# Performance work log

Measured on AMD Instinct MI355X. Metric: run time of the kernel, lower is better.

Reference implementation:

```python
import jax, jax.numpy as jnp
import numpy as np

N_NODES = 100000
N_EDGES = 600000
H_FEATS = 128


def setup_inputs() -> dict:
    key = jax.random.key(0)
    k_h, k_src, k_dst, k_w1, k_w2 = jax.random.split(key, 5)
    h = jax.random.normal(k_h, (N_NODES, H_FEATS), dtype=jnp.float32)
    src = jax.random.randint(k_src, (N_EDGES,), 0, N_NODES, dtype=jnp.int64)
    dst = jax.random.randint(k_dst, (N_EDGES,), 0, N_NODES, dtype=jnp.int64)
    # torch.nn.Linear-style params: out = x @ W.T + b
    W1_w = jax.random.normal(k_w1, (H_FEATS, 2 * H_FEATS), dtype=jnp.float32) * (1.0 / np.sqrt(2 * H_FEATS))
    W1_b = jnp.zeros((H_FEATS,), dtype=jnp.float32)
    W2_w = jax.random.normal(k_w2, (1, H_FEATS), dtype=jnp.float32) * (1.0 / np.sqrt(H_FEATS))
    W2_b = jnp.zeros((1,), dtype=jnp.float32)
    return {"h": h, "src": src, "dst": dst, "W1_w": W1_w, "W1_b": W1_b, "W2_w": W2_w, "W2_b": W2_b}


def reference(h, src, dst, W1_w, W1_b, W2_w, W2_b):
    # Gather endpoint features per edge and concatenate: [E, 2*h_feats]
    edge_feat = jnp.concatenate([h[src], h[dst]], axis=-1)
    # 2-layer MLP per edge: Linear -> ReLU -> Linear, scalar score per edge
    hid = jax.nn.relu(edge_feat @ W1_w.T + W1_b)  # [E, h_feats]
    score = hid @ W2_w.T + W2_b                   # [E, 1]
    return score[:, 0]                            # [E]
```

## Files before the change

kernel.cpp:

```cpp
#include <hip/hip_runtime.h>
#include <hip/hip_bf16.h>
#include <stdint.h>

typedef short bf16x8 __attribute__((ext_vector_type(8)));
typedef float f32x4  __attribute__((ext_vector_type(4)));

__device__ __forceinline__ ushort f2b(float f) {
  __hip_bfloat16 t = __float2bfloat16(f);
  return *reinterpret_cast<ushort*>(&t);
}
__device__ __forceinline__ bf16x8 pack8(float4 a, float4 b) {
  bf16x8 r;
  r[0]=(short)f2b(a.x); r[1]=(short)f2b(a.y); r[2]=(short)f2b(a.z); r[3]=(short)f2b(a.w);
  r[4]=(short)f2b(b.x); r[5]=(short)f2b(b.y); r[6]=(short)f2b(b.z); r[7]=(short)f2b(b.w);
  return r;
}

__global__ void repack_W1(const float* __restrict__ W1, int4* __restrict__ blob) {
  const int tid = blockIdx.x * 256 + threadIdx.x;
  const int l15  = tid & 15;
  const int lg   = (tid >> 4) & 3;
  const int kk   = (tid >> 6) & 3;
  const int nt   = (tid >> 8) & 7;
  const int half = (tid >> 11) & 1;
  const float* wp = W1 + (size_t)(nt * 16 + l15) * 256 + half * 128 + kk * 32 + lg * 8;
  const float4 fa = *(const float4*)wp;
  const float4 fb = *(const float4*)(wp + 4);
  bf16x8 r = pack8(fa, fb);
  blob[tid] = *reinterpret_cast<int4*>(&r);
}

__device__ __forceinline__ void lds_barrier() {
  asm volatile("s_waitcnt lgkmcnt(0)" ::: "memory");
  __builtin_amdgcn_sched_barrier(0);
  __builtin_amdgcn_s_barrier();
  __builtin_amdgcn_sched_barrier(0);
}

__global__ __launch_bounds__(256, 3) void node_uv(
    const float* __restrict__ h, const int4* __restrict__ blob,
    const float* __restrict__ b1,
    uint8_t* __restrict__ u8, uint8_t* __restrict__ v8,
    float* __restrict__ su, float* __restrict__ sv,
    int Nn, int NT, int nblocks, int niter)
{
  __shared__ ushort As[2][2048];

  const int t0   = threadIdx.x;
  const int w    = t0 >> 6;
  const int l    = t0 & 63;
  const int l15  = l & 15;
  const int lg   = l >> 4;
  const int half = w >> 1;
  const int hw   = w & 1;

  bf16x8 bfrag[4][4];
#pragma unroll
  for (int ntl = 0; ntl < 4; ++ntl)
#pragma unroll
    for (int kk = 0; kk < 4; ++kk) {
      int4 x = blob[((half * 8 + hw * 4 + ntl) * 4 + kk) * 64 + l];
      bfrag[ntl][kk] = *reinterpret_cast<bf16x8*>(&x);
    }

  float b1r[4];
#pragma unroll
  for (int ntl = 0; ntl < 4; ++ntl)
    b1r[ntl] = half ? 0.f : b1[hw * 64 + ntl * 16 + l15];

  uint8_t* __restrict__ outp = half ? v8 : u8;
  float*   __restrict__ outs = half ? sv : su;

  const float4* h4 = (const float4*)h;

#define LOADT(T, g)                                            \
  {                                                            \
    const size_t hb = (size_t)(T) * 512;                       \
    _Pragma("unroll")                                          \
    for (int k = 0; k < 2; ++k) {                              \
      const int i = k * 256 + t0;                              \
      const int gr = (T) * 16 + (i >> 5);                      \
      (g)[k] = h4[gr < Nn ? hb + i : 0];                       \
    }                                                          \
  }

#define STORET(b, g)                                           \
  {                                                            \
    _Pragma("unroll")                                          \
    for (int k = 0; k < 2; ++k) {                              \
      const int i = k * 256 + t0, row = i >> 5, c = i & 31;    \
      ushort4 o;                                               \
      o.x = f2b((g)[k].x); o.y = f2b((g)[k].y);                \
      o.z = f2b((g)[k].z); o.w = f2b((g)[k].w);                \
      *(ushort4*)(&As[b][row * 128 + (((c >> 1) ^ (row & 7)) << 3) + (c & 1) * 4]) = o; \
    }                                                          \
  }

  int tc = blockIdx.x;
  int tn = tc + nblocks;
  float4 gC[2], gN[2], gNN[2];
  LOADT(tc, gC);
  LOADT(tn, gN);
  STORET(0, gC);
  lds_barrier();
  int cur = 0;

  for (int it = 0; it < niter; ++it) {
    const int tnn = tn + nblocks;
    LOADT(tnn, gNN);
    STORET(cur ^ 1, gN);

    if (tc < NT) {
      f32x4 acc[4];
#pragma unroll
      for (int ntl = 0; ntl < 4; ++ntl) acc[ntl] = (f32x4){0.f, 0.f, 0.f, 0.f};

#pragma unroll
      for (int kk = 0; kk < 4; ++kk) {
        const int slot = (kk * 4 + lg) ^ (l15 & 7);
        int4 av = *(const int4*)(&As[cur][l15 * 128 + slot * 8]);
        const bf16x8 a = *reinterpret_cast<bf16x8*>(&av);
#pragma unroll
        for (int ntl = 0; ntl < 4; ++ntl)
          acc[ntl] = __builtin_amdgcn_mfma_f32_16x16x32_bf16(a, bfrag[ntl][kk], acc[ntl], 0, 0, 0);
      }

      const int n0 = tc * 16;
#pragma unroll
      for (int r = 0; r < 4; ++r) {
        float vals[4];
        float m = 1e-30f;
#pragma unroll
        for (int ntl = 0; ntl < 4; ++ntl) {
          const float x = acc[ntl][r] + b1r[ntl];
          vals[ntl] = x;
          m = fmaxf(m, fabsf(x));
        }
        m = fmaxf(m, __shfl_xor(m, 1));
        m = fmaxf(m, __shfl_xor(m, 2));
        m = fmaxf(m, __shfl_xor(m, 4));
        m = fmaxf(m, __shfl_xor(m, 8));
        const float inv = 127.0f * __builtin_amdgcn_rcpf(m);
        uint32_t pk = 0;
#pragma unroll
        for (int j = 0; j < 4; ++j) {
          const int q = (int)rintf(vals[j] * inv) + 128;
          pk |= (uint32_t)q << (8 * j);
        }
        const int node = n0 + lg * 4 + r;
        if (node < Nn) {
          *(uint32_t*)(outp + (size_t)node * 128 + l15 * 8 + hw * 4) = pk;
          if (l15 == 0) outs[node * 2 + hw] = m * (1.0f / 127.0f);
        }
      }
    }

    lds_barrier();
    tc = tn; tn = tnn;
    gN[0] = gNN[0]; gN[1] = gNN[1];
    cur ^= 1;
  }
#undef LOADT
#undef STORET
}

__global__ __launch_bounds__(256) void edge_score_i8(
    const uint8_t* __restrict__ u8, const uint8_t* __restrict__ v8,
    const float* __restrict__ su, const float* __restrict__ sv,
    const int* __restrict__ src, const int* __restrict__ dst,
    const float* __restrict__ w2, const float* __restrict__ b2p,
    float* __restrict__ out, int E)
{
  const int t  = threadIdx.x;
  const int l  = t & 63;
  const int q  = l & 15;
  const int lg = l >> 4;

  float w2r[8];
#pragma unroll
  for (int j = 0; j < 8; ++j) w2r[j] = w2[j * 16 + q];
  const float b2 = b2p[0];

  const int gw = blockIdx.x * 4 + (t >> 6);
  const int TW = gridDim.x * 4;
  const float2* su2 = (const float2*)su;
  const float2* sv2 = (const float2*)sv;

  for (int base = gw * 16; base < E; base += TW * 16) {
    int e[4]; bool ok[4];
    uint2 ug[4], vg[4];
    float2 ss[4], sd[4];
#pragma unroll
    for (int i = 0; i < 4; ++i) {
      e[i]  = base + i * 4 + lg;
      ok[i] = e[i] < E;
      const int eS = ok[i] ? e[i] : 0;
      const int s = src[eS];
      const int d = dst[eS];
      ug[i] = *(const uint2*)(u8 + (size_t)s * 128 + q * 8);
      vg[i] = *(const uint2*)(v8 + (size_t)d * 128 + q * 8);
      ss[i] = su2[s];
      sd[i] = sv2[d];
    }
#pragma unroll
    for (int i = 0; i < 4; ++i) {
      const uint32_t ux = ug[i].x, uy = ug[i].y;
      const uint32_t vx = vg[i].x, vy = vg[i].y;
      const float bse0 = -128.0f * (ss[i].x + sd[i].x);
      const float bse1 = -128.0f * (ss[i].y + sd[i].y);
      float acc = 0.f;
#pragma unroll
      for (int j = 0; j < 4; ++j) {
        const float cu = (float)((ux >> (8 * j)) & 0xffu);
        const float cv = (float)((vx >> (8 * j)) & 0xffu);
        float x = fmaf(cu, ss[i].x, fmaf(cv, sd[i].x, bse0));
        x = fmaxf(x, 0.f);
        acc = fmaf(x, w2r[j], acc);
      }
#pragma unroll
      for (int j = 0; j < 4; ++j) {
        const float cu = (float)((uy >> (8 * j)) & 0xffu);
        const float cv = (float)((vy >> (8 * j)) & 0xffu);
        float x = fmaf(cu, ss[i].y, fmaf(cv, sd[i].y, bse1));
        x = fmaxf(x, 0.f);
        acc = fmaf(x, w2r[4 + j], acc);
      }
      acc += __shfl_xor(acc, 1);
      acc += __shfl_xor(acc, 2);
      acc += __shfl_xor(acc, 4);
      acc += __shfl_xor(acc, 8);
      if (q == 0 && ok[i]) out[e[i]] = acc + b2;
    }
  }
}

extern "C" void kernel_launch(void* const* d_in, const int* in_sizes, int n_in,
                              void* d_out, int out_size, void* d_ws, size_t ws_size,
                              hipStream_t stream) {
  const float* h   = (const float*)d_in[0];
  const int*   src = (const int*)d_in[1];
  const int*   dst = (const int*)d_in[2];
  const float* W1  = (const float*)d_in[3];
  const float* b1  = (const float*)d_in[4];
  const float* w2  = (const float*)d_in[5];
  const float* b2  = (const float*)d_in[6];
  float* out = (float*)d_out;

  const int nh = in_sizes[0];
  const int Nn = nh / 128;
  const int E  = in_sizes[1];

  uint8_t* ws = (uint8_t*)d_ws;
  int4*  blob = (int4*)ws;
  size_t off  = 65536;
  float* su   = (float*)(ws + off);  off += (size_t)Nn * 8;
  off = (off + 511) & ~(size_t)511;
  float* sv   = (float*)(ws + off);  off += (size_t)Nn * 8;
  off = (off + 511) & ~(size_t)511;
  uint8_t* u8 = ws + off;            off += (size_t)Nn * 128;
  uint8_t* v8 = ws + off;

  hipLaunchKernelGGL(repack_W1, dim3(16), dim3(256), 0, stream, W1, blob);

  const int NT      = (Nn + 15) / 16;
  const int nblocks = 768;
  const int niter   = (NT + nblocks - 1) / nblocks;
  hipLaunchKernelGGL(node_uv, dim3(nblocks), dim3(256), 0, stream,
                     h, blob, b1, u8, v8, su, sv, Nn, NT, nblocks, niter);

  hipLaunchKernelGGL(edge_score_i8, dim3(3072), dim3(256), 0, stream,
                     u8, v8, su, sv, src, dst, w2, b2, out, E);
}
```

Measured before the change: 59.27 us.

## Fuse W1 repack, node projection and edge scoring into one cooperative kernel

Merges the three launches (W1 repack, per-node projection, per-edge scoring) into a single cooperative kernel. Each wave converts its W1 fragments to bf16 directly from fp32, and a grid-wide sync separates the node phase from the edge phase. The goal is to remove launch overheads and inter-kernel gaps. In exchange it adds a grid barrier, caps the edge phase at the occupancy-limited grid size (at most 1024 blocks instead of 3072), and raises the launch-bounds occupancy target, which may constrain registers.

```diff
diff --git a/kernel.cpp b/kernel.cpp
--- a/kernel.cpp
+++ b/kernel.cpp
@@ -1,6 +1,9 @@
 #include <hip/hip_runtime.h>
 #include <hip/hip_bf16.h>
+#include <hip/hip_cooperative_groups.h>
 #include <stdint.h>
+
+namespace cg = cooperative_groups;
 
 typedef short bf16x8 __attribute__((ext_vector_type(8)));
 typedef float f32x4  __attribute__((ext_vector_type(4)));
@@ -16,20 +19,6 @@
   return r;
 }
 
-__global__ void repack_W1(const float* __restrict__ W1, int4* __restrict__ blob) {
-  const int tid = blockIdx.x * 256 + threadIdx.x;
-  const int l15  = tid & 15;
-  const int lg   = (tid >> 4) & 3;
-  const int kk   = (tid >> 6) & 3;
-  const int nt   = (tid >> 8) & 7;
-  const int half = (tid >> 11) & 1;
-  const float* wp = W1 + (size_t)(nt * 16 + l15) * 256 + half * 128 + kk * 32 + lg * 8;
-  const float4 fa = *(const float4*)wp;
-  const float4 fb = *(const float4*)(wp + 4);
-  bf16x8 r = pack8(fa, fb);
-  blob[tid] = *reinterpret_cast<int4*>(&r);
-}
-
 __device__ __forceinline__ void lds_barrier() {
   asm volatile("s_waitcnt lgkmcnt(0)" ::: "memory");
   __builtin_amdgcn_sched_barrier(0);
@@ -37,12 +26,15 @@
   __builtin_amdgcn_sched_barrier(0);
 }
 
-__global__ __launch_bounds__(256, 3) void node_uv(
-    const float* __restrict__ h, const int4* __restrict__ blob,
-    const float* __restrict__ b1,
+__global__ __launch_bounds__(256, 4) void fused_mlp(
+    const float* __restrict__ h, const float* __restrict__ W1,
+    const float* __restrict__ b1, const float* __restrict__ w2,
+    const float* __restrict__ b2p,
+    const int* __restrict__ src, const int* __restrict__ dst,
     uint8_t* __restrict__ u8, uint8_t* __restrict__ v8,
     float* __restrict__ su, float* __restrict__ sv,
-    int Nn, int NT, int nblocks, int niter)
+    float* __restrict__ out,
+    int Nn, int NT, int E)
 {
   __shared__ ushort As[2][2048];
 
@@ -53,15 +45,21 @@
   const int lg   = l >> 4;
   const int half = w >> 1;
   const int hw   = w & 1;
+  const int nb   = gridDim.x;
+  const int niter = (NT + nb - 1) / nb;
 
   bf16x8 bfrag[4][4];
 #pragma unroll
-  for (int ntl = 0; ntl < 4; ++ntl)
+  for (int ntl = 0; ntl < 4; ++ntl) {
+    const int j = hw * 64 + ntl * 16 + l15;
+    const float* wp = W1 + (size_t)j * 256 + half * 128 + lg * 8;
 #pragma unroll
     for (int kk = 0; kk < 4; ++kk) {
-      int4 x = blob[((half * 8 + hw * 4 + ntl) * 4 + kk) * 64 + l];
-      bfrag[ntl][kk] = *reinterpret_cast<bf16x8*>(&x);
+      const float4 fa = *(const float4*)(wp + kk * 32);
+      const float4 fb = *(const float4*)(wp + kk * 32 + 4);
+      bfrag[ntl][kk] = pack8(fa, fb);
     }
+  }
 
   float b1r[4];
 #pragma unroll
@@ -96,140 +94,135 @@
     }                                                          \
   }
 
-  int tc = blockIdx.x;
-  int tn = tc + nblocks;
-  float4 gC[2], gN[2], gNN[2];
-  LOADT(tc, gC);
-  LOADT(tn, gN);
-  STORET(0, gC);
-  lds_barrier();
-  int cur = 0;
-
-  for (int it = 0; it < niter; ++it) {
-    const int tnn = tn + nblocks;
-    LOADT(tnn, gNN);
-    STORET(cur ^ 1, gN);
-
-    if (tc < NT) {
-      f32x4 acc[4];
-#pragma unroll
-      for (int ntl = 0; ntl < 4; ++ntl) acc[ntl] = (f32x4){0.f, 0.f, 0.f, 0.f};
-
-#pragma unroll
-      for (int kk = 0; kk < 4; ++kk) {
-        const int slot = (kk * 4 + lg) ^ (l15 & 7);
-        int4 av = *(const int4*)(&As[cur][l15 * 128 + slot * 8]);
-        const bf16x8 a = *reinterpret_cast<bf16x8*>(&av);
-#pragma unroll
-        for (int ntl = 0; ntl < 4; ++ntl)
-          acc[ntl] = __builtin_amdgcn_mfma_f32_16x16x32_bf16(a, bfrag[ntl][kk], acc[ntl], 0, 0, 0);
+  {
+    int tc = blockIdx.x;
+    int tn = tc + nb;
+    float4 gC[2], gN[2], gNN[2];
+    LOADT(tc, gC);
+    LOADT(tn, gN);
+    STORET(0, gC);
+    lds_barrier();
+    int cur = 0;
+
+    for (int it = 0; it < niter; ++it) {
+      const int tnn = tn + nb;
+      LOADT(tnn, gNN);
+      STORET(cur ^ 1, gN);
+
+      if (tc < NT) {
+        f32x4 acc[4];
+#pragma unroll
+        for (int ntl = 0; ntl < 4; ++ntl) acc[ntl] = (f32x4){0.f, 0.f, 0.f, 0.f};
+
+#pragma unroll
+        for (int kk = 0; kk < 4; ++kk) {
+          const int slot = (kk * 4 + lg) ^ (l15 & 7);
+          int4 av = *(const int4*)(&As[cur][l15 * 128 + slot * 8]);
+          const bf16x8 a = *reinterpret_cast<bf16x8*>(&av);
+#pragma unroll
+          for (int ntl = 0; ntl < 4; ++ntl)
+            acc[ntl] = __builtin_amdgcn_mfma_f32_16x16x32_bf16(a, bfrag[ntl][kk], acc[ntl], 0, 0, 0);
+        }
+
+        const int n0 = tc * 16;
+#pragma unroll
+        for (int r = 0; r < 4; ++r) {
+          float vals[4];
+          float m = 1e-30f;
+#pragma unroll
+          for (int ntl = 0; ntl < 4; ++ntl) {
+            const float x = acc[ntl][r] + b1r[ntl];
+            vals[ntl] = x;
+            m = fmaxf(m, fabsf(x));
+          }
+          m = fmaxf(m, __shfl_xor(m, 1));
+          m = fmaxf(m, __shfl_xor(m, 2));
+          m = fmaxf(m, __shfl_xor(m, 4));
+          m = fmaxf(m, __shfl_xor(m, 8));
+          const float inv = 127.0f * __builtin_amdgcn_rcpf(m);
+          uint32_t pk = 0;
+#pragma unroll
+          for (int j = 0; j < 4; ++j) {
+            const int q = (int)rintf(vals[j] * inv) + 128;
+            pk |= (uint32_t)q << (8 * j);
+          }
+          const int node = n0 + lg * 4 + r;
+          if (node < Nn) {
+            *(uint32_t*)(outp + (size_t)node * 128 + l15 * 8 + hw * 4) = pk;
+            if (l15 == 0) outs[node * 2 + hw] = m * (1.0f / 127.0f);
+          }
+        }
       }
 
-      const int n0 = tc * 16;
-#pragma unroll
-      for (int r = 0; r < 4; ++r) {
-        float vals[4];
-        float m = 1e-30f;
-#pragma unroll
-        for (int ntl = 0; ntl < 4; ++ntl) {
-          const float x = acc[ntl][r] + b1r[ntl];
-          vals[ntl] = x;
-          m = fmaxf(m, fabsf(x));
-        }
-        m = fmaxf(m, __shfl_xor(m, 1));
-        m = fmaxf(m, __shfl_xor(m, 2));
-        m = fmaxf(m, __shfl_xor(m, 4));
-        m = fmaxf(m, __shfl_xor(m, 8));
-        const float inv = 127.0f * __builtin_amdgcn_rcpf(m);
-        uint32_t pk = 0;
-#pragma unroll
-        for (int j = 0; j < 4; ++j) {
-          const int q = (int)rintf(vals[j] * inv) + 128;
-          pk |= (uint32_t)q << (8 * j);
-        }
-        const int node = n0 + lg * 4 + r;
-        if (node < Nn) {
-          *(uint32_t*)(outp + (size_t)node * 128 + l15 * 8 + hw * 4) = pk;
-          if (l15 == 0) outs[node * 2 + hw] = m * (1.0f / 127.0f);
-        }
-      }
+      lds_barrier();
+      tc = tn; tn = tnn;
+      gN[0] = gNN[0]; gN[1] = gNN[1];
+      cur ^= 1;
     }
-
-    lds_barrier();
-    tc = tn; tn = tnn;
-    gN[0] = gNN[0]; gN[1] = gNN[1];
-    cur ^= 1;
   }
 #undef LOADT
 #undef STORET
-}
-
-__global__ __launch_bounds__(256) void edge_score_i8(
-    const uint8_t* __restrict__ u8, const uint8_t* __restrict__ v8,
-    const float* __restrict__ su, const float* __restrict__ sv,
-    const int* __restrict__ src, const int* __restrict__ dst,
-    const float* __restrict__ w2, const float* __restrict__ b2p,
-    float* __restrict__ out, int E)
-{
-  const int t  = threadIdx.x;
-  const int l  = t & 63;
-  const int q  = l & 15;
-  const int lg = l >> 4;
-
-  float w2r[8];
-#pragma unroll
-  for (int j = 0; j < 8; ++j) w2r[j] = w2[j * 16 + q];
-  const float b2 = b2p[0];
-
-  const int gw = blockIdx.x * 4 + (t >> 6);
-  const int TW = gridDim.x * 4;
-  const float2* su2 = (const float2*)su;
-  const float2* sv2 = (const float2*)sv;
-
-  for (int base = gw * 16; base < E; base += TW * 16) {
-    int e[4]; bool ok[4];
-    uint2 ug[4], vg[4];
-    float2 ss[4], sd[4];
-#pragma unroll
-    for (int i = 0; i < 4; ++i) {
-      e[i]  = base + i * 4 + lg;
-      ok[i] = e[i] < E;
-      const int eS = ok[i] ? e[i] : 0;
-      const int s = src[eS];
-      const int d = dst[eS];
-      ug[i] = *(const uint2*)(u8 + (size_t)s * 128 + q * 8);
-      vg[i] = *(const uint2*)(v8 + (size_t)d * 128 + q * 8);
-      ss[i] = su2[s];
-      sd[i] = sv2[d];
-    }
-#pragma unroll
-    for (int i = 0; i < 4; ++i) {
-      const uint32_t ux = ug[i].x, uy = ug[i].y;
-      const uint32_t vx = vg[i].x, vy = vg[i].y;
-      const float bse0 = -128.0f * (ss[i].x + sd[i].x);
-      const float bse1 = -128.0f * (ss[i].y + sd[i].y);
-      float acc = 0.f;
-#pragma unroll
-      for (int j = 0; j < 4; ++j) {
-        const float cu = (float)((ux >> (8 * j)) & 0xffu);
-        const float cv = (float)((vx >> (8 * j)) & 0xffu);
-        float x = fmaf(cu, ss[i].x, fmaf(cv, sd[i].x, bse0));
-        x = fmaxf(x, 0.f);
-        acc = fmaf(x, w2r[j], acc);
+
+  __threadfence();
+  cg::this_grid().sync();
+
+  {
+    const int q = l15;
+    float w2r[8];
+#pragma unroll
+    for (int j = 0; j < 8; ++j) w2r[j] = w2[j * 16 + q];
+    const float b2 = b2p[0];
+
+    const int gw = blockIdx.x * 4 + w;
+    const int TW = nb * 4;
+    const float2* su2 = (const float2*)su;
+    const float2* sv2 = (const float2*)sv;
+
+    for (int base = gw * 16; base < E; base += TW * 16) {
+      int e[4]; bool ok[4];
+      uint2 ug[4], vg[4];
+      float2 ss[4], sd[4];
+#pragma unroll
+      for (int i = 0; i < 4; ++i) {
+        e[i]  = base + i * 4 + lg;
+        ok[i] = e[i] < E;
+        const int eS = ok[i] ? e[i] : 0;
+        const int s = src[eS];
+        const int d = dst[eS];
+        ug[i] = *(const uint2*)(u8 + (size_t)s * 128 + q * 8);
+        vg[i] = *(const uint2*)(v8 + (size_t)d * 128 + q * 8);
+        ss[i] = su2[s];
+        sd[i] = sv2[d];
       }
 #pragma unroll
-      for (int j = 0; j < 4; ++j) {
-        const float cu = (float)((uy >> (8 * j)) & 0xffu);
-        const float cv = (float)((vy >> (8 * j)) & 0xffu);
-        float x = fmaf(cu, ss[i].y, fmaf(cv, sd[i].y, bse1));
-        x = fmaxf(x, 0.f);
-        acc = fmaf(x, w2r[4 + j], acc);
+      for (int i = 0; i < 4; ++i) {
+        const uint32_t ux = ug[i].x, uy = ug[i].y;
+        const uint32_t vx = vg[i].x, vy = vg[i].y;
+        const float bse0 = -128.0f * (ss[i].x + sd[i].x);
+        const float bse1 = -128.0f * (ss[i].y + sd[i].y);
+        float acc = 0.f;
+#pragma unroll
+        for (int j = 0; j < 4; ++j) {
+          const float cu = (float)((ux >> (8 * j)) & 0xffu);
+          const float cv = (float)((vx >> (8 * j)) & 0xffu);
+          float x = fmaf(cu, ss[i].x, fmaf(cv, sd[i].x, bse0));
+          x = fmaxf(x, 0.f);
+          acc = fmaf(x, w2r[j], acc);
+        }
+#pragma unroll
+        for (int j = 0; j < 4; ++j) {
+          const float cu = (float)((uy >> (8 * j)) & 0xffu);
+          const float cv = (float)((vy >> (8 * j)) & 0xffu);
+          float x = fmaf(cu, ss[i].y, fmaf(cv, sd[i].y, bse1));
+          x = fmaxf(x, 0.f);
+          acc = fmaf(x, w2r[4 + j], acc);
+        }
+        acc += __shfl_xor(acc, 1);
+        acc += __shfl_xor(acc, 2);
+        acc += __shfl_xor(acc, 4);
+        acc += __shfl_xor(acc, 8);
+        if (q == 0 && ok[i]) out[e[i]] = acc + b2;
       }
-      acc += __shfl_xor(acc, 1);
-      acc += __shfl_xor(acc, 2);
-      acc += __shfl_xor(acc, 4);
-      acc += __shfl_xor(acc, 8);
-      if (q == 0 && ok[i]) out[e[i]] = acc + b2;
     }
   }
 }
@@ -251,8 +244,7 @@
   const int E  = in_sizes[1];
 
   uint8_t* ws = (uint8_t*)d_ws;
-  int4*  blob = (int4*)ws;
-  size_t off  = 65536;
+  size_t off  = 0;
   float* su   = (float*)(ws + off);  off += (size_t)Nn * 8;
   off = (off + 511) & ~(size_t)511;
   float* sv   = (float*)(ws + off);  off += (size_t)Nn * 8;
@@ -260,14 +252,19 @@
   uint8_t* u8 = ws + off;            off += (size_t)Nn * 128;
   uint8_t* v8 = ws + off;
 
-  hipLaunchKernelGGL(repack_W1, dim3(16), dim3(256), 0, stream, W1, blob);
-
-  const int NT      = (Nn + 15) / 16;
-  const int nblocks = 768;
-  const int niter   = (NT + nblocks - 1) / nblocks;
-  hipLaunchKernelGGL(node_uv, dim3(nblocks), dim3(256), 0, stream,
-                     h, blob, b1, u8, v8, su, sv, Nn, NT, nblocks, niter);
-
-  hipLaunchKernelGGL(edge_score_i8, dim3(3072), dim3(256), 0, stream,
-                     u8, v8, su, sv, src, dst, w2, b2, out, E);
-}
+  const int NT = (Nn + 15) / 16;
+
+  int maxb = 4;
+  (void)hipOccupancyMaxActiveBlocksPerMultiprocessor(&maxb, fused_mlp, 256, 0);
+  int grid = maxb * 256;
+  if (grid > 1024) grid = 1024;
+  if (grid < 256)  grid = 256;
+
+  int nn = Nn, nt = NT, e = E;
+  void* args[] = { (void*)&h, (void*)&W1, (void*)&b1, (void*)&w2, (void*)&b2,
+                   (void*)&src, (void*)&dst, (void*)&u8, (void*)&v8,
+                   (void*)&su, (void*)&sv, (void*)&out,
+                   (void*)&nn, (void*)&nt, (void*)&e };
+  hipLaunchCooperativeKernel((const void*)fused_mlp, dim3(grid), dim3(256),
+                             args, 0, stream);
+}
```

New measurement: 213.7 us. +260.5%, slower.

## Bucket edges by source range so edge blocks hit L2-local node rows

Applied to the files above, without the earlier changes.

Adds extra blocks to the node projection kernel that bin edge indices into 8 buckets by source-node range, using LDS histograms and global atomics. The edge scoring kernel then assigns each block to one bucket, so the u8 gathers for that block touch a narrower node range and may stay in the per-XCD L2. Loads of v8 become nontemporal to limit cache pollution. The cost is an extra indirection through the bucket array, an unordered scatter of output writes, and a workspace of 8*E ints.

```diff
diff --git a/kernel.cpp b/kernel.cpp
--- a/kernel.cpp
+++ b/kernel.cpp
@@ -4,6 +4,7 @@
 
 typedef short bf16x8 __attribute__((ext_vector_type(8)));
 typedef float f32x4  __attribute__((ext_vector_type(4)));
+typedef uint32_t u32x2 __attribute__((ext_vector_type(2)));
 
 __device__ __forceinline__ ushort f2b(float f) {
   __hip_bfloat16 t = __float2bfloat16(f);
@@ -16,7 +17,16 @@
   return r;
 }
 
-__global__ void repack_W1(const float* __restrict__ W1, int4* __restrict__ blob) {
+__device__ __forceinline__ void lds_barrier() {
+  asm volatile("s_waitcnt lgkmcnt(0)" ::: "memory");
+  __builtin_amdgcn_sched_barrier(0);
+  __builtin_amdgcn_s_barrier();
+  __builtin_amdgcn_sched_barrier(0);
+}
+
+__global__ void repack_W1(const float* __restrict__ W1, int4* __restrict__ blob,
+                          int* __restrict__ gcnt) {
+  if (blockIdx.x == 0 && threadIdx.x < 8) gcnt[threadIdx.x] = 0;
   const int tid = blockIdx.x * 256 + threadIdx.x;
   const int l15  = tid & 15;
   const int lg   = (tid >> 4) & 3;
@@ -30,23 +40,46 @@
   blob[tid] = *reinterpret_cast<int4*>(&r);
 }
 
-__device__ __forceinline__ void lds_barrier() {
-  asm volatile("s_waitcnt lgkmcnt(0)" ::: "memory");
-  __builtin_amdgcn_sched_barrier(0);
-  __builtin_amdgcn_s_barrier();
-  __builtin_amdgcn_sched_barrier(0);
-}
-
-__global__ __launch_bounds__(256, 3) void node_uv(
+__global__ __launch_bounds__(256, 3) void node_uv_bucket(
     const float* __restrict__ h, const int4* __restrict__ blob,
     const float* __restrict__ b1,
     uint8_t* __restrict__ u8, uint8_t* __restrict__ v8,
     float* __restrict__ su, float* __restrict__ sv,
-    int Nn, int NT, int nblocks, int niter)
+    int Nn, int NT, int nb, int niter,
+    const int* __restrict__ src, int* __restrict__ bkt, int* __restrict__ gcnt,
+    int E, unsigned Mdiv)
 {
   __shared__ ushort As[2][2048];
-
-  const int t0   = threadIdx.x;
+  __shared__ int lh[8], lb[8], lh2[8];
+
+  const int t0 = threadIdx.x;
+
+  if ((int)blockIdx.x >= nb) {
+    const int j  = blockIdx.x - nb;
+    const int C  = (E + 255) >> 8;
+    const int e0 = j * C;
+    const int e1 = (e0 + C) < E ? (e0 + C) : E;
+    if (t0 < 8) { lh[t0] = 0; lh2[t0] = 0; }
+    __syncthreads();
+    for (int e = e0 + t0; e < e1; e += 256) {
+      const unsigned s = (unsigned)src[e];
+      int sh = (int)(((unsigned long long)s * Mdiv) >> 34);
+      if (sh > 7) sh = 7;
+      atomicAdd(&lh[sh], 1);
+    }
+    __syncthreads();
+    if (t0 < 8) lb[t0] = atomicAdd(&gcnt[t0], lh[t0]);
+    __syncthreads();
+    for (int e = e0 + t0; e < e1; e += 256) {
+      const unsigned s = (unsigned)src[e];
+      int sh = (int)(((unsigned long long)s * Mdiv) >> 34);
+      if (sh > 7) sh = 7;
+      const int r = atomicAdd(&lh2[sh], 1);
+      bkt[(size_t)sh * E + lb[sh] + r] = e;
+    }
+    return;
+  }
+
   const int w    = t0 >> 6;
   const int l    = t0 & 63;
   const int l15  = l & 15;
@@ -97,7 +130,7 @@
   }
 
   int tc = blockIdx.x;
-  int tn = tc + nblocks;
+  int tn = tc + nb;
   float4 gC[2], gN[2], gNN[2];
   LOADT(tc, gC);
   LOADT(tn, gN);
@@ -106,7 +139,7 @@
   int cur = 0;
 
   for (int it = 0; it < niter; ++it) {
-    const int tnn = tn + nblocks;
+    const int tnn = tn + nb;
     LOADT(tnn, gNN);
     STORET(cur ^ 1, gN);
 
@@ -143,9 +176,9 @@
         const float inv = 127.0f * __builtin_amdgcn_rcpf(m);
         uint32_t pk = 0;
 #pragma unroll
-        for (int j = 0; j < 4; ++j) {
-          const int q = (int)rintf(vals[j] * inv) + 128;
-          pk |= (uint32_t)q << (8 * j);
+        for (int jj = 0; jj < 4; ++jj) {
+          const int q = (int)rintf(vals[jj] * inv) + 128;
+          pk |= (uint32_t)q << (8 * jj);
         }
         const int node = n0 + lg * 4 + r;
         if (node < Nn) {
@@ -164,10 +197,11 @@
 #undef STORET
 }
 
-__global__ __launch_bounds__(256) void edge_score_i8(
+__global__ __launch_bounds__(256) void edge_score_shard(
     const uint8_t* __restrict__ u8, const uint8_t* __restrict__ v8,
     const float* __restrict__ su, const float* __restrict__ sv,
     const int* __restrict__ src, const int* __restrict__ dst,
+    const int* __restrict__ bkt, const int* __restrict__ gcnt,
     const float* __restrict__ w2, const float* __restrict__ b2p,
     float* __restrict__ out, int E)
 {
@@ -175,37 +209,44 @@
   const int l  = t & 63;
   const int q  = l & 15;
   const int lg = l >> 4;
+  const int w  = t >> 6;
 
   float w2r[8];
 #pragma unroll
   for (int j = 0; j < 8; ++j) w2r[j] = w2[j * 16 + q];
   const float b2 = b2p[0];
 
-  const int gw = blockIdx.x * 4 + (t >> 6);
-  const int TW = gridDim.x * 4;
+  const int bucket = blockIdx.x & 7;
+  const int bj     = blockIdx.x >> 3;
+  const int NBJ    = gridDim.x >> 3;
+  const int cnt    = gcnt[bucket];
+  if (cnt == 0) return;
+  const int* p = bkt + (size_t)bucket * E;
+
   const float2* su2 = (const float2*)su;
   const float2* sv2 = (const float2*)sv;
 
-  for (int base = gw * 16; base < E; base += TW * 16) {
-    int e[4]; bool ok[4];
-    uint2 ug[4], vg[4];
+  for (int base = (bj * 4 + w) * 16; base < cnt; base += NBJ * 64) {
+    int ee[4]; bool ok[4];
+    uint2 ug[4]; u32x2 vg[4];
     float2 ss[4], sd[4];
 #pragma unroll
     for (int i = 0; i < 4; ++i) {
-      e[i]  = base + i * 4 + lg;
-      ok[i] = e[i] < E;
-      const int eS = ok[i] ? e[i] : 0;
-      const int s = src[eS];
-      const int d = dst[eS];
+      const int idx = base + i * 4 + lg;
+      ok[i] = idx < cnt;
+      const int idc = ok[i] ? idx : cnt - 1;
+      ee[i] = p[idc];
+      const int s = src[ee[i]];
+      const int d = dst[ee[i]];
       ug[i] = *(const uint2*)(u8 + (size_t)s * 128 + q * 8);
-      vg[i] = *(const uint2*)(v8 + (size_t)d * 128 + q * 8);
+      vg[i] = __builtin_nontemporal_load((const u32x2*)(v8 + (size_t)d * 128 + q * 8));
       ss[i] = su2[s];
       sd[i] = sv2[d];
     }
 #pragma unroll
     for (int i = 0; i < 4; ++i) {
       const uint32_t ux = ug[i].x, uy = ug[i].y;
-      const uint32_t vx = vg[i].x, vy = vg[i].y;
+      const uint32_t vx = vg[i][0], vy = vg[i][1];
       const float bse0 = -128.0f * (ss[i].x + sd[i].x);
       const float bse1 = -128.0f * (ss[i].y + sd[i].y);
       float acc = 0.f;
@@ -229,7 +270,7 @@
       acc += __shfl_xor(acc, 2);
       acc += __shfl_xor(acc, 4);
       acc += __shfl_xor(acc, 8);
-      if (q == 0 && ok[i]) out[e[i]] = acc + b2;
+      if (q == 0 && ok[i]) out[ee[i]] = acc + b2;
     }
   }
 }
@@ -253,21 +294,28 @@
   uint8_t* ws = (uint8_t*)d_ws;
   int4*  blob = (int4*)ws;
   size_t off  = 65536;
+  int*  gcnt  = (int*)(ws + off);    off += 512;
   float* su   = (float*)(ws + off);  off += (size_t)Nn * 8;
   off = (off + 511) & ~(size_t)511;
   float* sv   = (float*)(ws + off);  off += (size_t)Nn * 8;
   off = (off + 511) & ~(size_t)511;
   uint8_t* u8 = ws + off;            off += (size_t)Nn * 128;
-  uint8_t* v8 = ws + off;
-
-  hipLaunchKernelGGL(repack_W1, dim3(16), dim3(256), 0, stream, W1, blob);
+  uint8_t* v8 = ws + off;            off += (size_t)Nn * 128;
+  off = (off + 511) & ~(size_t)511;
+  int*   bkt  = (int*)(ws + off);
+
+  const unsigned div  = (unsigned)((Nn + 7) / 8);
+  const unsigned Mdiv = (unsigned)((((unsigned long long)1 << 34) + div - 1) / div);
+
+  hipLaunchKernelGGL(repack_W1, dim3(16), dim3(256), 0, stream, W1, blob, gcnt);
 
   const int NT      = (Nn + 15) / 16;
   const int nblocks = 768;
   const int niter   = (NT + nblocks - 1) / nblocks;
-  hipLaunchKernelGGL(node_uv, dim3(nblocks), dim3(256), 0, stream,
-                     h, blob, b1, u8, v8, su, sv, Nn, NT, nblocks, niter);
-
-  hipLaunchKernelGGL(edge_score_i8, dim3(3072), dim3(256), 0, stream,
-                     u8, v8, su, sv, src, dst, w2, b2, out, E);
-}
+  hipLaunchKernelGGL(node_uv_bucket, dim3(nblocks + 256), dim3(256), 0, stream,
+                     h, blob, b1, u8, v8, su, sv, Nn, NT, nblocks, niter,
+                     src, bkt, gcnt, E, Mdiv);
+
+  hipLaunchKernelGGL(edge_score_shard, dim3(2048), dim3(256), 0, stream,
+                     u8, v8, su, sv, src, dst, bkt, gcnt, w2, b2, out, E);
+}
```

New measurement: 77.99 us. +31.6%, slower.
